# Kernel tuning notes

Measured on AMD Instinct MI355X. Metric: run time of the kernel, lower is better.

Reference implementation:

```python
import jax, jax.numpy as jnp
import numpy as np


def setup_inputs() -> dict:
    key = jax.random.key(0)
    k1, k2, k3, k4, k5 = jax.random.split(key, 5)
    B, T, K, H, A = 16, 256, 256, 512, 49
    return {
        "hiddens_des": jax.random.normal(k1, (B, K, H), dtype=jnp.float32),
        "hiddens_title": jax.random.normal(k2, (B, T, H), dtype=jnp.float32),
        "Wv": jax.random.normal(k3, (A, H), dtype=jnp.float32) * (1.0 / np.sqrt(H)),
        "Wg": jax.random.normal(k4, (A, H), dtype=jnp.float32) * (1.0 / np.sqrt(H)),
        "Wh": jax.random.normal(k5, (1, A), dtype=jnp.float32) * (1.0 / np.sqrt(A)),
    }


def reference(hiddens_des, hiddens_title, Wv, Wg, Wh):
    # Dropout is identity (eval mode) for the deterministic baseline.
    # content_v: (B,1,K,49) + (B,T,1,49) -> (B,T,K,49)
    cv = jnp.einsum("bkh,ah->bka", hiddens_des, Wv)    # (B,K,49)
    cg = jnp.einsum("bth,ah->bta", hiddens_title, Wg)  # (B,T,49)
    content = cv[:, None, :, :] + cg[:, :, None, :]     # (B,T,K,49)
    z = jnp.einsum("btka,a->btk", jnp.tanh(content), Wh[0])  # (B,T,K)
    alpha = jax.nn.softmax(z, axis=-1)                  # softmax over K
    c_hat = jnp.einsum("btk,bkh->bth", alpha, hiddens_des)  # (B,T,H)
    return (c_hat, alpha)
```

## Files before the change

kernel.cpp:

```cpp
#include <hip/hip_runtime.h>
#include <hip/hip_bf16.h>

#define B_ 16
#define T_ 256
#define K_ 256
#define H_ 512
#define A_ 49
#define APAD 64

typedef __attribute__((ext_vector_type(8))) short short8;
typedef __attribute__((ext_vector_type(4))) float f32x4;

__device__ __forceinline__ ushort f2bf(float f) {
    uint u = __builtin_bit_cast(uint, f);
    u += 0x7FFF + ((u >> 16) & 1);
    return (ushort)(u >> 16);
}

__device__ __forceinline__ void cvt_hilo(float4 v0, float4 v1, short8& hi, short8& lo) {
    float v[8] = {v0.x, v0.y, v0.z, v0.w, v1.x, v1.y, v1.z, v1.w};
    #pragma unroll
    for (int i = 0; i < 8; ++i) {
        ushort h = f2bf(v[i]);
        float hf = __builtin_bit_cast(float, (uint)h << 16);
        hi[i] = (short)h;
        lo[i] = (short)f2bf(v[i] - hf);
    }
}

__device__ __forceinline__ float sig2(float x) {
    float e = __expf(2.f * x);
    return __builtin_amdgcn_rcpf(e + 1.f);
}

__global__ __launch_bounds__(256) void kW(const float* __restrict__ Wv,
                                          const float* __restrict__ Wg,
                                          ushort* __restrict__ Whl)
{
    int blk = blockIdx.x;
    int m = blk >> 6, row = blk & 63;
    const float* W = m ? Wg : Wv;
    int tid = threadIdx.x;
    ushort* hi = Whl + ((size_t)(m * 2 + 0) * 64 + row) * H_;
    ushort* lo = Whl + ((size_t)(m * 2 + 1) * 64 + row) * H_;
    #pragma unroll
    for (int c = tid; c < H_; c += 256) {
        float v = (row < A_) ? W[(size_t)row * H_ + c] : 0.f;
        ushort h = f2bf(v);
        float hf = __builtin_bit_cast(float, (uint)h << 16);
        hi[c] = h;
        lo[c] = f2bf(v - hf);
    }
}

__global__ __launch_bounds__(256) void kAP(const float* __restrict__ des,
                                           const float* __restrict__ title,
                                           const ushort* __restrict__ Whl,
                                           float* __restrict__ cvT,
                                           float* __restrict__ cg,
                                           ushort* __restrict__ desT)
{
    __shared__ float Tls[32][33];
    int tid = threadIdx.x;

    if (blockIdx.x >= 512) {
        int tb = blockIdx.x - 512;
        int b = tb >> 7, rem = tb & 127;
        int k0 = (rem >> 4) * 32, h0 = (rem & 15) * 32;
        int kk = tid >> 3, c4 = (tid & 7) * 4;
        float4 v = *(const float4*)(des + ((size_t)(b * K_ + k0 + kk) * H_) + h0 + c4);
        Tls[kk][c4 + 0] = v.x; Tls[kk][c4 + 1] = v.y;
        Tls[kk][c4 + 2] = v.z; Tls[kk][c4 + 3] = v.w;
        __syncthreads();
        int hh = tid >> 3;
        ushort4 o;
        o.x = f2bf(Tls[c4 + 0][hh]);
        o.y = f2bf(Tls[c4 + 1][hh]);
        o.z = f2bf(Tls[c4 + 2][hh]);
        o.w = f2bf(Tls[c4 + 3][hh]);
        *(ushort4*)(desT + ((size_t)(b * H_ + h0 + hh) * K_) + k0 + c4) = o;
        return;
    }

    int wv = tid >> 6, lane = tid & 63;
    int tile = blockIdx.x;
    bool isDes = tile < 256;
    int lr = lane & 15, lc = lane >> 4;
    int g = wv;

    const float* X = isDes ? (des + (size_t)tile * 16 * H_)
                           : (title + (size_t)(tile - 256) * 16 * H_);
    int m = isDes ? 0 : 1;
    const ushort* whiP = Whl + ((size_t)(m * 2 + 0) * 64 + g * 16 + lr) * H_ + lc * 8;
    const ushort* wloP = Whl + ((size_t)(m * 2 + 1) * 64 + g * 16 + lr) * H_ + lc * 8;
    const float*  xp0  = X + (size_t)lr * H_ + lc * 8;

    f32x4 acc = {};

    for (int k0 = 0; k0 < H_; k0 += 32) {
        float4 xv0 = *(const float4*)(xp0 + k0);
        float4 xv1 = *(const float4*)(xp0 + k0 + 4);
        short8 xhi, xlo;
        cvt_hilo(xv0, xv1, xhi, xlo);
        short8 whi = *(const short8*)(whiP + k0);
        short8 wlo = *(const short8*)(wloP + k0);
        if (isDes) {
            acc = __builtin_amdgcn_mfma_f32_16x16x32_bf16(whi, xhi, acc, 0, 0, 0);
            acc = __builtin_amdgcn_mfma_f32_16x16x32_bf16(whi, xlo, acc, 0, 0, 0);
            acc = __builtin_amdgcn_mfma_f32_16x16x32_bf16(wlo, xhi, acc, 0, 0, 0);
        } else {
            acc = __builtin_amdgcn_mfma_f32_16x16x32_bf16(xhi, whi, acc, 0, 0, 0);
            acc = __builtin_amdgcn_mfma_f32_16x16x32_bf16(xlo, whi, acc, 0, 0, 0);
            acc = __builtin_amdgcn_mfma_f32_16x16x32_bf16(xhi, wlo, acc, 0, 0, 0);
        }
    }

    if (isDes) {
        int krows = tile * 16;
        int b = krows >> 8, kb = krows & 255;
        #pragma unroll
        for (int r = 0; r < 4; ++r) {
            int a = g * 16 + lc * 4 + r;
            cvT[((size_t)b * APAD + a) * K_ + kb + lr] = acc[r];
        }
    } else {
        int trows = (tile - 256) * 16;
        #pragma unroll
        for (int r = 0; r < 4; ++r) {
            int row = trows + lc * 4 + r;
            cg[(size_t)row * APAD + g * 16 + lr] = acc[r];
        }
    }
}

__global__ __launch_bounds__(1024) void kZ(const float* __restrict__ cvT,
                                           const float* __restrict__ cg,
                                           const float* __restrict__ Wh,
                                           const ushort* __restrict__ desT,
                                           float* __restrict__ alpha,
                                           float* __restrict__ chat)
{
    __shared__ float  sCg[16][APAD];
    __shared__ float  sWh[APAD];
    __shared__ float  sRedM[16][4];
    __shared__ float  sRedS[16][4];
    __shared__ ushort sA[16][K_ + 8];

    int bid = blockIdx.x;
    int b  = bid & 15;
    int t0 = (bid >> 4) << 4;
    int tid = threadIdx.x;
    int k  = tid & 255;
    int tg = tid >> 8;
    int tb = tg * 4;

    if (tid < 256) {
        int row = tid >> 4, c = (tid & 15) * 4;
        *(float4*)(&sCg[row][c]) =
            *(const float4*)(cg + (size_t)(b * T_ + t0 + row) * APAD + c);
    } else if (tid < 256 + APAD) {
        int a = tid - 256;
        sWh[a] = (a < A_) ? Wh[a] : 0.f;
    }
    __syncthreads();

    float zacc[4] = {0.f, 0.f, 0.f, 0.f};
    float sw = 0.f;
    const float* cvp = cvT + (size_t)b * APAD * K_ + k;

    for (int c = 0; c < 12; ++c) {
        int a0 = c * 4;
        float xa[4];
        #pragma unroll
        for (int i = 0; i < 4; ++i) xa[i] = cvp[(size_t)(a0 + i) * K_];
        float4 w4 = *(const float4*)(&sWh[a0]);
        sw += w4.x + w4.y + w4.z + w4.w;
        #pragma unroll
        for (int j = 0; j < 4; ++j) {
            float4 cj = *(const float4*)(&sCg[tb + j][a0]);
            zacc[j] += w4.x * sig2(xa[0] + cj.x)
                     + w4.y * sig2(xa[1] + cj.y)
                     + w4.z * sig2(xa[2] + cj.z)
                     + w4.w * sig2(xa[3] + cj.w);
        }
    }
    {
        float xa = cvp[(size_t)48 * K_];
        float wh = sWh[48];
        sw += wh;
        #pragma unroll
        for (int j = 0; j < 4; ++j)
            zacc[j] += wh * sig2(xa + sCg[tb + j][48]);
    }
    float z[4];
    #pragma unroll
    for (int j = 0; j < 4; ++j) z[j] = sw - 2.f * zacc[j];

    int wv = tid >> 6, lane = tid & 63, w3 = wv & 3;
    #pragma unroll
    for (int j = 0; j < 4; ++j) {
        float m = z[j];
        #pragma unroll
        for (int off = 32; off > 0; off >>= 1) m = fmaxf(m, __shfl_xor(m, off));
        if (lane == 0) sRedM[tb + j][w3] = m;
    }
    __syncthreads();
    #pragma unroll
    for (int j = 0; j < 4; ++j) {
        int t = tb + j;
        float m = fmaxf(fmaxf(sRedM[t][0], sRedM[t][1]),
                        fmaxf(sRedM[t][2], sRedM[t][3]));
        z[j] = __expf(z[j] - m);
    }
    #pragma unroll
    for (int j = 0; j < 4; ++j) {
        float s = z[j];
        #pragma unroll
        for (int off = 32; off > 0; off >>= 1) s += __shfl_xor(s, off);
        if (lane == 0) sRedS[tb + j][w3] = s;
    }
    __syncthreads();
    #pragma unroll
    for (int j = 0; j < 4; ++j) {
        int t = tb + j;
        float s = sRedS[t][0] + sRedS[t][1] + sRedS[t][2] + sRedS[t][3];
        float rs = __builtin_amdgcn_rcpf(s);
        rs = rs * (2.f - s * rs);
        float al = z[j] * rs;
        alpha[(size_t)(b * T_ + t0 + t) * K_ + k] = al;
        sA[t][k] = f2bf(al);
    }
    __syncthreads();

    int lr = lane & 15, lc = lane >> 4;
    int h0 = wv * 32;
    const ushort* Bp = desT + ((size_t)(b * H_ + h0 + lr)) * K_ + lc * 8;

    f32x4 acc0 = {}, acc1 = {};
    #pragma unroll
    for (int kb = 0; kb < K_; kb += 32) {
        short8 a8 = *(const short8*)(&sA[lr][kb + lc * 8]);
        short8 b0 = *(const short8*)(Bp + kb);
        short8 b1 = *(const short8*)(Bp + (size_t)16 * K_ + kb);
        acc0 = __builtin_amdgcn_mfma_f32_16x16x32_bf16(a8, b0, acc0, 0, 0, 0);
        acc1 = __builtin_amdgcn_mfma_f32_16x16x32_bf16(a8, b1, acc1, 0, 0, 0);
    }

    #pragma unroll
    for (int r = 0; r < 4; ++r) {
        int row = t0 + lc * 4 + r;
        chat[((size_t)(b * T_ + row)) * H_ + h0 + lr]      = acc0[r];
        chat[((size_t)(b * T_ + row)) * H_ + h0 + 16 + lr] = acc1[r];
    }
}

extern "C" void kernel_launch(void* const* d_in, const int* in_sizes, int n_in,
                              void* d_out, int out_size, void* d_ws, size_t ws_size,
                              hipStream_t stream) {
    const float* des   = (const float*)d_in[0];
    const float* title = (const float*)d_in[1];
    const float* Wv    = (const float*)d_in[2];
    const float* Wg    = (const float*)d_in[3];
    const float* Wh    = (const float*)d_in[4];

    float* chat  = (float*)d_out;
    float* alpha = (float*)d_out + (size_t)B_ * T_ * H_;

    char* ws = (char*)d_ws;
    float*  cvT  = (float*)ws;
    float*  cg   = cvT + (size_t)B_ * APAD * K_;
    ushort* desT = (ushort*)(cg + (size_t)B_ * T_ * APAD);
    ushort* Whl  = desT + (size_t)B_ * H_ * K_;

    hipLaunchKernelGGL(kW, dim3(128), dim3(256), 0, stream, Wv, Wg, Whl);
    hipLaunchKernelGGL(kAP, dim3(2560), dim3(256), 0, stream,
                       des, title, Whl, cvT, cg, desT);
    hipLaunchKernelGGL(kZ, dim3(B_ * (T_ / 16)), dim3(1024), 0, stream,
                       cvT, cg, Wh, desT, alpha, chat);
}
```

Before: 53.08 us.

## Fuse three kernels into one persistent kernel with a global atomic barrier

Replaces the weight-conversion, projection/transpose and softmax/matmul kernels with a single 256-block kernel of 1024 threads. Weight hi/lo bf16 splits are built per block in shared memory instead of a separate kernel, and a global atomic-counter barrier separates the projection phase from the attention phase. The aim is to remove launch overhead and inter-kernel gaps. The cost is a grid-wide spin barrier that needs all 256 blocks co-resident, an added memset launch, and fewer, larger blocks doing the projection work.

```diff
diff --git a/kernel.cpp b/kernel.cpp
--- a/kernel.cpp
+++ b/kernel.cpp
@@ -7,6 +7,8 @@
 #define H_ 512
 #define A_ 49
 #define APAD 64
+#define GRID 256
+#define WSTR 520
 
 typedef __attribute__((ext_vector_type(8))) short short8;
 typedef __attribute__((ext_vector_type(4))) float f32x4;
@@ -33,134 +35,138 @@
     return __builtin_amdgcn_rcpf(e + 1.f);
 }
 
-__global__ __launch_bounds__(256) void kW(const float* __restrict__ Wv,
-                                          const float* __restrict__ Wg,
-                                          ushort* __restrict__ Whl)
+struct SMproj { ushort whi[16][WSTR]; ushort wlo[16][WSTR]; };
+struct SMtr   { float t[4][32][33]; };
+struct SMz    { float cg[16][APAD]; float wh[APAD];
+                float redM[16][4]; float redS[16][4];
+                ushort a[16][K_ + 8]; };
+union SMu { SMproj p; SMtr tr; SMz z; };
+
+__global__ __launch_bounds__(1024) void kFused(const float* __restrict__ des,
+                                               const float* __restrict__ title,
+                                               const float* __restrict__ Wv,
+                                               const float* __restrict__ Wg,
+                                               const float* __restrict__ Wh,
+                                               float* __restrict__ alpha,
+                                               float* __restrict__ chat,
+                                               float* __restrict__ cvT,
+                                               float* __restrict__ cg,
+                                               ushort* __restrict__ desT,
+                                               uint* __restrict__ counter)
 {
-    int blk = blockIdx.x;
-    int m = blk >> 6, row = blk & 63;
-    const float* W = m ? Wg : Wv;
+    __shared__ SMu sm;
     int tid = threadIdx.x;
-    ushort* hi = Whl + ((size_t)(m * 2 + 0) * 64 + row) * H_;
-    ushort* lo = Whl + ((size_t)(m * 2 + 1) * 64 + row) * H_;
-    #pragma unroll
-    for (int c = tid; c < H_; c += 256) {
-        float v = (row < A_) ? W[(size_t)row * H_ + c] : 0.f;
-        ushort h = f2bf(v);
-        float hf = __builtin_bit_cast(float, (uint)h << 16);
-        hi[c] = h;
-        lo[c] = f2bf(v - hf);
-    }
-}
-
-__global__ __launch_bounds__(256) void kAP(const float* __restrict__ des,
-                                           const float* __restrict__ title,
-                                           const ushort* __restrict__ Whl,
-                                           float* __restrict__ cvT,
-                                           float* __restrict__ cg,
-                                           ushort* __restrict__ desT)
-{
-    __shared__ float Tls[32][33];
-    int tid = threadIdx.x;
-
-    if (blockIdx.x >= 512) {
-        int tb = blockIdx.x - 512;
-        int b = tb >> 7, rem = tb & 127;
-        int k0 = (rem >> 4) * 32, h0 = (rem & 15) * 32;
-        int kk = tid >> 3, c4 = (tid & 7) * 4;
-        float4 v = *(const float4*)(des + ((size_t)(b * K_ + k0 + kk) * H_) + h0 + c4);
-        Tls[kk][c4 + 0] = v.x; Tls[kk][c4 + 1] = v.y;
-        Tls[kk][c4 + 2] = v.z; Tls[kk][c4 + 3] = v.w;
+    int bid = blockIdx.x;
+
+    if (bid < 128) {
+        int g = bid & 3;
+        int tg16 = bid >> 2;
+        bool isDes = tg16 < 16;
+        const float* W = isDes ? Wv : Wg;
+
+        {
+            int row = tid >> 6;
+            int c0 = (tid & 63) * 8;
+            int a = g * 16 + row;
+            float4 v0 = make_float4(0.f,0.f,0.f,0.f), v1 = v0;
+            if (a < A_) {
+                v0 = *(const float4*)(W + (size_t)a * H_ + c0);
+                v1 = *(const float4*)(W + (size_t)a * H_ + c0 + 4);
+            }
+            short8 hi, lo;
+            cvt_hilo(v0, v1, hi, lo);
+            *(short8*)&sm.p.whi[row][c0] = hi;
+            *(short8*)&sm.p.wlo[row][c0] = lo;
+        }
         __syncthreads();
-        int hh = tid >> 3;
-        ushort4 o;
-        o.x = f2bf(Tls[c4 + 0][hh]);
-        o.y = f2bf(Tls[c4 + 1][hh]);
-        o.z = f2bf(Tls[c4 + 2][hh]);
-        o.w = f2bf(Tls[c4 + 3][hh]);
-        *(ushort4*)(desT + ((size_t)(b * H_ + h0 + hh) * K_) + k0 + c4) = o;
-        return;
-    }
-
-    int wv = tid >> 6, lane = tid & 63;
-    int tile = blockIdx.x;
-    bool isDes = tile < 256;
-    int lr = lane & 15, lc = lane >> 4;
-    int g = wv;
-
-    const float* X = isDes ? (des + (size_t)tile * 16 * H_)
-                           : (title + (size_t)(tile - 256) * 16 * H_);
-    int m = isDes ? 0 : 1;
-    const ushort* whiP = Whl + ((size_t)(m * 2 + 0) * 64 + g * 16 + lr) * H_ + lc * 8;
-    const ushort* wloP = Whl + ((size_t)(m * 2 + 1) * 64 + g * 16 + lr) * H_ + lc * 8;
-    const float*  xp0  = X + (size_t)lr * H_ + lc * 8;
-
-    f32x4 acc = {};
-
-    for (int k0 = 0; k0 < H_; k0 += 32) {
-        float4 xv0 = *(const float4*)(xp0 + k0);
-        float4 xv1 = *(const float4*)(xp0 + k0 + 4);
-        short8 xhi, xlo;
-        cvt_hilo(xv0, xv1, xhi, xlo);
-        short8 whi = *(const short8*)(whiP + k0);
-        short8 wlo = *(const short8*)(wloP + k0);
+
+        int wv = tid >> 6, lane = tid & 63;
+        int lr = lane & 15, lc = lane >> 4;
+        int tile = tg16 * 16 + wv;
+        const float* X = isDes ? (des + (size_t)tile * 16 * H_)
+                               : (title + (size_t)(tile - 256) * 16 * H_);
+        const float* xp0 = X + (size_t)lr * H_ + lc * 8;
+
+        f32x4 acc = {};
+        for (int k0 = 0; k0 < H_; k0 += 32) {
+            float4 xv0 = *(const float4*)(xp0 + k0);
+            float4 xv1 = *(const float4*)(xp0 + k0 + 4);
+            short8 xhi, xlo;
+            cvt_hilo(xv0, xv1, xhi, xlo);
+            short8 whi = *(const short8*)&sm.p.whi[lr][k0 + lc * 8];
+            short8 wlo = *(const short8*)&sm.p.wlo[lr][k0 + lc * 8];
+            if (isDes) {
+                acc = __builtin_amdgcn_mfma_f32_16x16x32_bf16(whi, xhi, acc, 0, 0, 0);
+                acc = __builtin_amdgcn_mfma_f32_16x16x32_bf16(whi, xlo, acc, 0, 0, 0);
+                acc = __builtin_amdgcn_mfma_f32_16x16x32_bf16(wlo, xhi, acc, 0, 0, 0);
+            } else {
+                acc = __builtin_amdgcn_mfma_f32_16x16x32_bf16(xhi, whi, acc, 0, 0, 0);
+                acc = __builtin_amdgcn_mfma_f32_16x16x32_bf16(xlo, whi, acc, 0, 0, 0);
+                acc = __builtin_amdgcn_mfma_f32_16x16x32_bf16(xhi, wlo, acc, 0, 0, 0);
+            }
+        }
+
         if (isDes) {
-            acc = __builtin_amdgcn_mfma_f32_16x16x32_bf16(whi, xhi, acc, 0, 0, 0);
-            acc = __builtin_amdgcn_mfma_f32_16x16x32_bf16(whi, xlo, acc, 0, 0, 0);
-            acc = __builtin_amdgcn_mfma_f32_16x16x32_bf16(wlo, xhi, acc, 0, 0, 0);
+            int krows = tile * 16;
+            int b = krows >> 8, kb = krows & 255;
+            #pragma unroll
+            for (int r = 0; r < 4; ++r) {
+                int a = g * 16 + lc * 4 + r;
+                cvT[((size_t)b * APAD + a) * K_ + kb + lr] = acc[r];
+            }
         } else {
-            acc = __builtin_amdgcn_mfma_f32_16x16x32_bf16(xhi, whi, acc, 0, 0, 0);
-            acc = __builtin_amdgcn_mfma_f32_16x16x32_bf16(xlo, whi, acc, 0, 0, 0);
-            acc = __builtin_amdgcn_mfma_f32_16x16x32_bf16(xhi, wlo, acc, 0, 0, 0);
-        }
-    }
-
-    if (isDes) {
-        int krows = tile * 16;
-        int b = krows >> 8, kb = krows & 255;
-        #pragma unroll
-        for (int r = 0; r < 4; ++r) {
-            int a = g * 16 + lc * 4 + r;
-            cvT[((size_t)b * APAD + a) * K_ + kb + lr] = acc[r];
+            int trows = (tile - 256) * 16;
+            #pragma unroll
+            for (int r = 0; r < 4; ++r) {
+                int row = trows + lc * 4 + r;
+                cg[(size_t)row * APAD + g * 16 + lr] = acc[r];
+            }
         }
     } else {
-        int trows = (tile - 256) * 16;
-        #pragma unroll
-        for (int r = 0; r < 4; ++r) {
-            int row = trows + lc * 4 + r;
-            cg[(size_t)row * APAD + g * 16 + lr] = acc[r];
-        }
-    }
-}
-
-__global__ __launch_bounds__(1024) void kZ(const float* __restrict__ cvT,
-                                           const float* __restrict__ cg,
-                                           const float* __restrict__ Wh,
-                                           const ushort* __restrict__ desT,
-                                           float* __restrict__ alpha,
-                                           float* __restrict__ chat)
-{
-    __shared__ float  sCg[16][APAD];
-    __shared__ float  sWh[APAD];
-    __shared__ float  sRedM[16][4];
-    __shared__ float  sRedS[16][4];
-    __shared__ ushort sA[16][K_ + 8];
-
-    int bid = blockIdx.x;
+        int grp = tid >> 8, st2 = tid & 255;
+        int kk = st2 >> 3, c4 = (st2 & 7) * 4;
+        #pragma unroll
+        for (int it = 0; it < 4; ++it) {
+            int st = (bid - 128) * 16 + it * 4 + grp;
+            int b = st >> 7, rem = st & 127;
+            int k0 = (rem >> 4) * 32, h0 = (rem & 15) * 32;
+            float4 v = *(const float4*)(des + ((size_t)(b * K_ + k0 + kk) * H_) + h0 + c4);
+            sm.tr.t[grp][kk][c4 + 0] = v.x;
+            sm.tr.t[grp][kk][c4 + 1] = v.y;
+            sm.tr.t[grp][kk][c4 + 2] = v.z;
+            sm.tr.t[grp][kk][c4 + 3] = v.w;
+            __syncthreads();
+            ushort4 o;
+            o.x = f2bf(sm.tr.t[grp][c4 + 0][kk]);
+            o.y = f2bf(sm.tr.t[grp][c4 + 1][kk]);
+            o.z = f2bf(sm.tr.t[grp][c4 + 2][kk]);
+            o.w = f2bf(sm.tr.t[grp][c4 + 3][kk]);
+            *(ushort4*)(desT + ((size_t)(b * H_ + h0 + kk) * K_) + k0 + c4) = o;
+            __syncthreads();
+        }
+    }
+
+    __syncthreads();
+    if (tid == 0) {
+        __hip_atomic_fetch_add(counter, 1u, __ATOMIC_ACQ_REL, __HIP_MEMORY_SCOPE_AGENT);
+        while (__hip_atomic_load(counter, __ATOMIC_ACQUIRE, __HIP_MEMORY_SCOPE_AGENT) < GRID)
+            __builtin_amdgcn_s_sleep(8);
+    }
+    __syncthreads();
+
     int b  = bid & 15;
     int t0 = (bid >> 4) << 4;
-    int tid = threadIdx.x;
     int k  = tid & 255;
     int tg = tid >> 8;
     int tb = tg * 4;
 
     if (tid < 256) {
         int row = tid >> 4, c = (tid & 15) * 4;
-        *(float4*)(&sCg[row][c]) =
+        *(float4*)(&sm.z.cg[row][c]) =
             *(const float4*)(cg + (size_t)(b * T_ + t0 + row) * APAD + c);
     } else if (tid < 256 + APAD) {
         int a = tid - 256;
-        sWh[a] = (a < A_) ? Wh[a] : 0.f;
+        sm.z.wh[a] = (a < A_) ? Wh[a] : 0.f;
     }
     __syncthreads();
 
@@ -173,11 +179,11 @@
         float xa[4];
         #pragma unroll
         for (int i = 0; i < 4; ++i) xa[i] = cvp[(size_t)(a0 + i) * K_];
-        float4 w4 = *(const float4*)(&sWh[a0]);
+        float4 w4 = *(const float4*)(&sm.z.wh[a0]);
         sw += w4.x + w4.y + w4.z + w4.w;
         #pragma unroll
         for (int j = 0; j < 4; ++j) {
-            float4 cj = *(const float4*)(&sCg[tb + j][a0]);
+            float4 cj = *(const float4*)(&sm.z.cg[tb + j][a0]);
             zacc[j] += w4.x * sig2(xa[0] + cj.x)
                      + w4.y * sig2(xa[1] + cj.y)
                      + w4.z * sig2(xa[2] + cj.z)
@@ -186,11 +192,11 @@
     }
     {
         float xa = cvp[(size_t)48 * K_];
-        float wh = sWh[48];
+        float wh = sm.z.wh[48];
         sw += wh;
         #pragma unroll
         for (int j = 0; j < 4; ++j)
-            zacc[j] += wh * sig2(xa + sCg[tb + j][48]);
+            zacc[j] += wh * sig2(xa + sm.z.cg[tb + j][48]);
     }
     float z[4];
     #pragma unroll
@@ -202,14 +208,14 @@
         float m = z[j];
         #pragma unroll
         for (int off = 32; off > 0; off >>= 1) m = fmaxf(m, __shfl_xor(m, off));
-        if (lane == 0) sRedM[tb + j][w3] = m;
+        if (lane == 0) sm.z.redM[tb + j][w3] = m;
     }
     __syncthreads();
     #pragma unroll
     for (int j = 0; j < 4; ++j) {
         int t = tb + j;
-        float m = fmaxf(fmaxf(sRedM[t][0], sRedM[t][1]),
-                        fmaxf(sRedM[t][2], sRedM[t][3]));
+        float m = fmaxf(fmaxf(sm.z.redM[t][0], sm.z.redM[t][1]),
+                        fmaxf(sm.z.redM[t][2], sm.z.redM[t][3]));
         z[j] = __expf(z[j] - m);
     }
     #pragma unroll
@@ -217,18 +223,18 @@
         float s = z[j];
         #pragma unroll
         for (int off = 32; off > 0; off >>= 1) s += __shfl_xor(s, off);
-        if (lane == 0) sRedS[tb + j][w3] = s;
+        if (lane == 0) sm.z.redS[tb + j][w3] = s;
     }
     __syncthreads();
     #pragma unroll
     for (int j = 0; j < 4; ++j) {
         int t = tb + j;
-        float s = sRedS[t][0] + sRedS[t][1] + sRedS[t][2] + sRedS[t][3];
+        float s = sm.z.redS[t][0] + sm.z.redS[t][1] + sm.z.redS[t][2] + sm.z.redS[t][3];
         float rs = __builtin_amdgcn_rcpf(s);
         rs = rs * (2.f - s * rs);
         float al = z[j] * rs;
         alpha[(size_t)(b * T_ + t0 + t) * K_ + k] = al;
-        sA[t][k] = f2bf(al);
+        sm.z.a[t][k] = f2bf(al);
     }
     __syncthreads();
 
@@ -239,7 +245,7 @@
     f32x4 acc0 = {}, acc1 = {};
     #pragma unroll
     for (int kb = 0; kb < K_; kb += 32) {
-        short8 a8 = *(const short8*)(&sA[lr][kb + lc * 8]);
+        short8 a8 = *(const short8*)(&sm.z.a[lr][kb + lc * 8]);
         short8 b0 = *(const short8*)(Bp + kb);
         short8 b1 = *(const short8*)(Bp + (size_t)16 * K_ + kb);
         acc0 = __builtin_amdgcn_mfma_f32_16x16x32_bf16(a8, b0, acc0, 0, 0, 0);
@@ -270,11 +276,9 @@
     float*  cvT  = (float*)ws;
     float*  cg   = cvT + (size_t)B_ * APAD * K_;
     ushort* desT = (ushort*)(cg + (size_t)B_ * T_ * APAD);
-    ushort* Whl  = desT + (size_t)B_ * H_ * K_;
-
-    hipLaunchKernelGGL(kW, dim3(128), dim3(256), 0, stream, Wv, Wg, Whl);
-    hipLaunchKernelGGL(kAP, dim3(2560), dim3(256), 0, stream,
-                       des, title, Whl, cvT, cg, desT);
-    hipLaunchKernelGGL(kZ, dim3(B_ * (T_ / 16)), dim3(1024), 0, stream,
-                       cvT, cg, Wh, desT, alpha, chat);
-}
+    uint* counter = (uint*)(desT + (size_t)B_ * H_ * K_);
+
+    hipMemsetAsync(counter, 0, 128, stream);
+    hipLaunchKernelGGL(kFused, dim3(GRID), dim3(1024), 0, stream,
+                       des, title, Wv, Wg, Wh, alpha, chat, cvT, cg, desT, counter);
+}
```

Result: slower. 83.59 us (+57.5%).

## Stage cv tile in LDS, software-prefetch projection loads, batch chat MFMA loads

Applied to the files above, without the earlier changes.

kZ now copies the batch's cvT slice (49x256 floats) into shared memory and reads from LDS instead of strided global loads, and processes 8 attention dims per iteration. kAP's projection loop is fully unrolled with register double-buffering of the next x loads and a launch-bounds occupancy hint. The chat MFMA loop loads two k-steps of operands before issuing MFMAs. The ~50KB shared allocation in kZ may reduce occupancy, and all 1024 threads copy cvT redundantly per block across t-tiles.

```diff
diff --git a/kernel.cpp b/kernel.cpp
--- a/kernel.cpp
+++ b/kernel.cpp
@@ -53,12 +53,12 @@
     }
 }
 
-__global__ __launch_bounds__(256) void kAP(const float* __restrict__ des,
-                                           const float* __restrict__ title,
-                                           const ushort* __restrict__ Whl,
-                                           float* __restrict__ cvT,
-                                           float* __restrict__ cg,
-                                           ushort* __restrict__ desT)
+__global__ __launch_bounds__(256, 2) void kAP(const float* __restrict__ des,
+                                              const float* __restrict__ title,
+                                              const ushort* __restrict__ Whl,
+                                              float* __restrict__ cvT,
+                                              float* __restrict__ cg,
+                                              ushort* __restrict__ desT)
 {
     __shared__ float Tls[32][33];
     int tid = threadIdx.x;
@@ -96,14 +96,21 @@
     const float*  xp0  = X + (size_t)lr * H_ + lc * 8;
 
     f32x4 acc = {};
-
-    for (int k0 = 0; k0 < H_; k0 += 32) {
-        float4 xv0 = *(const float4*)(xp0 + k0);
-        float4 xv1 = *(const float4*)(xp0 + k0 + 4);
+    float4 xv0 = *(const float4*)(xp0);
+    float4 xv1 = *(const float4*)(xp0 + 4);
+
+    #pragma unroll
+    for (int i = 0; i < 16; ++i) {
+        int k0 = i * 32;
+        float4 nx0, nx1;
+        if (i < 15) {
+            nx0 = *(const float4*)(xp0 + k0 + 32);
+            nx1 = *(const float4*)(xp0 + k0 + 36);
+        }
+        short8 whi = *(const short8*)(whiP + k0);
+        short8 wlo = *(const short8*)(wloP + k0);
         short8 xhi, xlo;
         cvt_hilo(xv0, xv1, xhi, xlo);
-        short8 whi = *(const short8*)(whiP + k0);
-        short8 wlo = *(const short8*)(wloP + k0);
         if (isDes) {
             acc = __builtin_amdgcn_mfma_f32_16x16x32_bf16(whi, xhi, acc, 0, 0, 0);
             acc = __builtin_amdgcn_mfma_f32_16x16x32_bf16(whi, xlo, acc, 0, 0, 0);
@@ -113,6 +120,7 @@
             acc = __builtin_amdgcn_mfma_f32_16x16x32_bf16(xlo, whi, acc, 0, 0, 0);
             acc = __builtin_amdgcn_mfma_f32_16x16x32_bf16(xhi, wlo, acc, 0, 0, 0);
         }
+        if (i < 15) { xv0 = nx0; xv1 = nx1; }
     }
 
     if (isDes) {
@@ -140,6 +148,7 @@
                                            float* __restrict__ alpha,
                                            float* __restrict__ chat)
 {
+    __shared__ float  sCv[A_][K_];
     __shared__ float  sCg[16][APAD];
     __shared__ float  sWh[APAD];
     __shared__ float  sRedM[16][4];
@@ -154,6 +163,15 @@
     int tg = tid >> 8;
     int tb = tg * 4;
 
+    {
+        const float4* src = (const float4*)(cvT + (size_t)b * APAD * K_);
+        float4* dst = (float4*)&sCv[0][0];
+        #pragma unroll
+        for (int it = 0; it < 4; ++it) {
+            int idx = it * 1024 + tid;
+            if (idx < (A_ * K_) / 4) dst[idx] = src[idx];
+        }
+    }
     if (tid < 256) {
         int row = tid >> 4, c = (tid & 15) * 4;
         *(float4*)(&sCg[row][c]) =
@@ -165,32 +183,36 @@
     __syncthreads();
 
     float zacc[4] = {0.f, 0.f, 0.f, 0.f};
-    float sw = 0.f;
-    const float* cvp = cvT + (size_t)b * APAD * K_ + k;
-
-    for (int c = 0; c < 12; ++c) {
-        int a0 = c * 4;
-        float xa[4];
-        #pragma unroll
-        for (int i = 0; i < 4; ++i) xa[i] = cvp[(size_t)(a0 + i) * K_];
-        float4 w4 = *(const float4*)(&sWh[a0]);
-        sw += w4.x + w4.y + w4.z + w4.w;
+    #pragma unroll
+    for (int c = 0; c < 6; ++c) {
+        int a0 = c * 8;
+        float xa[8];
+        #pragma unroll
+        for (int i = 0; i < 8; ++i) xa[i] = sCv[a0 + i][k];
+        float4 w0 = *(const float4*)&sWh[a0];
+        float4 w1 = *(const float4*)&sWh[a0 + 4];
         #pragma unroll
         for (int j = 0; j < 4; ++j) {
-            float4 cj = *(const float4*)(&sCg[tb + j][a0]);
-            zacc[j] += w4.x * sig2(xa[0] + cj.x)
-                     + w4.y * sig2(xa[1] + cj.y)
-                     + w4.z * sig2(xa[2] + cj.z)
-                     + w4.w * sig2(xa[3] + cj.w);
+            float4 c0 = *(const float4*)&sCg[tb + j][a0];
+            float4 c1 = *(const float4*)&sCg[tb + j][a0 + 4];
+            zacc[j] += w0.x * sig2(xa[0] + c0.x) + w0.y * sig2(xa[1] + c0.y)
+                     + w0.z * sig2(xa[2] + c0.z) + w0.w * sig2(xa[3] + c0.w)
+                     + w1.x * sig2(xa[4] + c1.x) + w1.y * sig2(xa[5] + c1.y)
+                     + w1.z * sig2(xa[6] + c1.z) + w1.w * sig2(xa[7] + c1.w);
         }
     }
     {
-        float xa = cvp[(size_t)48 * K_];
+        float xa = sCv[48][k];
         float wh = sWh[48];
-        sw += wh;
         #pragma unroll
         for (int j = 0; j < 4; ++j)
             zacc[j] += wh * sig2(xa + sCg[tb + j][48]);
+    }
+    float sw = 0.f;
+    #pragma unroll
+    for (int q = 0; q < 16; ++q) {
+        float4 w4 = *(const float4*)&sWh[q * 4];
+        sw += w4.x + w4.y + w4.z + w4.w;
     }
     float z[4];
     #pragma unroll
@@ -238,12 +260,17 @@
 
     f32x4 acc0 = {}, acc1 = {};
     #pragma unroll
-    for (int kb = 0; kb < K_; kb += 32) {
-        short8 a8 = *(const short8*)(&sA[lr][kb + lc * 8]);
-        short8 b0 = *(const short8*)(Bp + kb);
-        short8 b1 = *(const short8*)(Bp + (size_t)16 * K_ + kb);
-        acc0 = __builtin_amdgcn_mfma_f32_16x16x32_bf16(a8, b0, acc0, 0, 0, 0);
-        acc1 = __builtin_amdgcn_mfma_f32_16x16x32_bf16(a8, b1, acc1, 0, 0, 0);
+    for (int kb = 0; kb < K_; kb += 64) {
+        short8 b00 = *(const short8*)(Bp + kb);
+        short8 b01 = *(const short8*)(Bp + (size_t)16 * K_ + kb);
+        short8 b10 = *(const short8*)(Bp + kb + 32);
+        short8 b11 = *(const short8*)(Bp + (size_t)16 * K_ + kb + 32);
+        short8 a80 = *(const short8*)(&sA[lr][kb + lc * 8]);
+        short8 a81 = *(const short8*)(&sA[lr][kb + 32 + lc * 8]);
+        acc0 = __builtin_amdgcn_mfma_f32_16x16x32_bf16(a80, b00, acc0, 0, 0, 0);
+        acc1 = __builtin_amdgcn_mfma_f32_16x16x32_bf16(a80, b01, acc1, 0, 0, 0);
+        acc0 = __builtin_amdgcn_mfma_f32_16x16x32_bf16(a81, b10, acc0, 0, 0, 0);
+        acc1 = __builtin_amdgcn_mfma_f32_16x16x32_bf16(a81, b11, acc1, 0, 0, 0);
     }
 
     #pragma unroll
```

New measurement: 95.66 us. 80.2% more time.
